# Kernel tuning notes

Measured on AMD Instinct MI355X. Metric: run time of the kernel, lower is better.

The kernel has to match this reference:

```python
import math
import jax, jax.numpy as jnp
import numpy as np

D_MODEL = 1024
NUM_HEADS = 16
D_HEAD = D_MODEL // NUM_HEADS  # 64
K_S = 32  # sparse top-k keys kept per query
B, N = 2, 2048


def setup_inputs() -> dict:
    key = jax.random.key(0)
    ks = jax.random.split(key, 9)
    s = 1.0 / math.sqrt(D_MODEL)
    return {
        "x": jax.random.normal(ks[0], (B, N, D_MODEL), dtype=jnp.float32),
        "Wq": jax.random.normal(ks[1], (D_MODEL, D_MODEL), dtype=jnp.float32) * s,
        "bq": jnp.zeros((D_MODEL,), dtype=jnp.float32),
        "Wk": jax.random.normal(ks[2], (D_MODEL, D_MODEL), dtype=jnp.float32) * s,
        "bk": jnp.zeros((D_MODEL,), dtype=jnp.float32),
        "Wv": jax.random.normal(ks[3], (D_MODEL, D_MODEL), dtype=jnp.float32) * s,
        "bv": jnp.zeros((D_MODEL,), dtype=jnp.float32),
        "Wo": jax.random.normal(ks[4], (D_MODEL, D_MODEL), dtype=jnp.float32) * s,
        "bo": jnp.zeros((D_MODEL,), dtype=jnp.float32),
    }


def _attn(x, Wq, bq, Wk, bk, Wv, bv, Wo, bo):
    b, n, _ = x.shape
    # projections (torch Linear: y = x W^T + b)
    q = (x @ Wq.T + bq).reshape(b, n, NUM_HEADS, D_HEAD).transpose(0, 2, 1, 3)
    k = (x @ Wk.T + bk).reshape(b, n, NUM_HEADS, D_HEAD).transpose(0, 2, 1, 3)
    v = (x @ Wv.T + bv).reshape(b, n, NUM_HEADS, D_HEAD).transpose(0, 2, 1, 3)
    # full scores [b, H, n, n]
    scores = jnp.einsum("bhqd,bhkd->bhqk", q, k) / math.sqrt(D_HEAD)
    # causal mask (triu above diagonal -> -inf)
    causal = jnp.triu(jnp.ones((n, n), dtype=bool), k=1)
    neg_inf = jnp.array(-jnp.inf, dtype=scores.dtype)
    scores = jnp.where(causal, neg_inf, scores)
    # sparse top-k: keep only K_S largest scores per query row
    vals, idx = jax.lax.top_k(scores, K_S)
    masked = jnp.full_like(scores, -jnp.inf)
    masked = jnp.put_along_axis(masked, idx, vals, axis=-1, inplace=False)
    attn = jax.nn.softmax(masked, axis=-1)  # dropout p=0.0 -> identity
    out = jnp.einsum("bhqk,bhkd->bhqd", attn, v)
    out = out.transpose(0, 2, 1, 3).reshape(b, n, D_MODEL)
    y = out @ Wo.T + bo
    return y, attn.mean(axis=1)


def reference(x, Wq, bq, Wk, bk, Wv, bv, Wo, bo):
    return _attn(x, Wq, bq, Wk, bk, Wv, bv, Wo, bo)
```

## Files before the change

kernel.cpp:

```cpp
#include <hip/hip_runtime.h>
#include <hip/hip_bf16.h>
#include <math.h>

#define BATCH   2
#define NTOK    2048
#define DMODEL  1024
#define HEADS   16
#define DHEAD   64
#define KSEL    32
#define MROWS   (BATCH * NTOK)

typedef short     bf16x8 __attribute__((ext_vector_type(8)));
typedef float     f32x4  __attribute__((ext_vector_type(4)));
typedef unsigned short ushort_t;
typedef unsigned long long u64;

#define GLOAD_LDS16(g, l) \
    __builtin_amdgcn_global_load_lds((const __attribute__((address_space(1))) void*)(g), \
                                     (__attribute__((address_space(3))) void*)(l), 16, 0, 0)

__device__ __forceinline__ ushort_t f2bf(float f) {
    unsigned u = __float_as_uint(f);
    unsigned r = (u + 0x7FFFu + ((u >> 16) & 1u)) >> 16;
    return (ushort_t)r;
}
__device__ __forceinline__ float bf2f(ushort_t h) {
    return __uint_as_float(((unsigned)h) << 16);
}

__global__ __launch_bounds__(256) void conv_split(const float* __restrict__ in,
                                                  ushort_t* __restrict__ hi,
                                                  ushort_t* __restrict__ lo, int n)
{
    const int i = (blockIdx.x * 256 + threadIdx.x) * 4;
    if (i + 3 < n) {
        const float4 v = *(const float4*)(in + i);
        ushort4 ph, pl;
        ph.x = f2bf(v.x); pl.x = f2bf(v.x - bf2f(ph.x));
        ph.y = f2bf(v.y); pl.y = f2bf(v.y - bf2f(ph.y));
        ph.z = f2bf(v.z); pl.z = f2bf(v.z - bf2f(ph.z));
        ph.w = f2bf(v.w); pl.w = f2bf(v.w - bf2f(ph.w));
        *(ushort4*)(hi + i) = ph;
        *(ushort4*)(lo + i) = pl;
    }
}

__global__ __launch_bounds__(256) void zero_fill(float* __restrict__ p, int n4)
{
    const int i = blockIdx.x * 256 + threadIdx.x;
    if (i < n4) ((float4*)p)[i] = (float4){0.f, 0.f, 0.f, 0.f};
}

__device__ __forceinline__ unsigned mono_key(float f) {
    const unsigned u = __float_as_uint(f);
    return (u ^ (unsigned)(((int)u >> 31) | 0x80000000)) + 1u;
}
__device__ __forceinline__ float unmono(unsigned m) {
    const unsigned u = m - 1u;
    return __uint_as_float(u ^ (unsigned)(((int)(~u) >> 31) | 0x80000000));
}

__global__ __launch_bounds__(256) void gemm_split_mfma(const ushort_t* __restrict__ Ahi,
                                                       const ushort_t* __restrict__ Alo,
                                                       const ushort_t* __restrict__ Bhi,
                                                       const ushort_t* __restrict__ Blo,
                                                       const float* __restrict__ bias,
                                                       float* __restrict__ out,
                                                       ushort_t* __restrict__ oh,
                                                       ushort_t* __restrict__ om,
                                                       ushort_t* __restrict__ ol,
                                                       int mode)
{
    __shared__ ushort_t AbufH[128 * 32];
    __shared__ ushort_t AbufL[128 * 32];
    __shared__ ushort_t BbufH[64 * 32];
    __shared__ ushort_t BbufL[64 * 32];

    const int tid  = threadIdx.x;
    const int wave = tid >> 6;
    const int lane = tid & 63;
    const int m0 = blockIdx.x * 128;
    const int n0 = blockIdx.y * 64;

    f32x4 acc[2][4];
#pragma unroll
    for (int i = 0; i < 2; ++i)
#pragma unroll
        for (int j = 0; j < 4; ++j) acc[i][j] = (f32x4){0.f, 0.f, 0.f, 0.f};

    const int ar0 = tid >> 2;
    const int ar1 = 64 + (tid >> 2);
    const int ak  = (tid & 3) << 3;
    const int br  = tid >> 2;

    const int fr = lane & 15;
    const int fk = (lane >> 4) << 3;

    for (int k0 = 0; k0 < DMODEL; k0 += 32) {
        __syncthreads();
        const size_t aoff0 = (size_t)(m0 + ar0) * DMODEL + k0 + ak;
        const size_t aoff1 = (size_t)(m0 + ar1) * DMODEL + k0 + ak;
        const size_t boff  = (size_t)(n0 + br) * DMODEL + k0 + ak;
        GLOAD_LDS16(Ahi + aoff0, AbufH + (size_t)tid * 8);
        GLOAD_LDS16(Ahi + aoff1, AbufH + (size_t)(256 + tid) * 8);
        GLOAD_LDS16(Alo + aoff0, AbufL + (size_t)tid * 8);
        GLOAD_LDS16(Alo + aoff1, AbufL + (size_t)(256 + tid) * 8);
        GLOAD_LDS16(Bhi + boff, BbufH + (size_t)tid * 8);
        GLOAD_LDS16(Blo + boff, BbufL + (size_t)tid * 8);
        __syncthreads();

        bf16x8 afh[2], afl[2], bfh[4], bfl[4];
#pragma unroll
        for (int mi = 0; mi < 2; ++mi) {
            const int ro = (wave * 32 + mi * 16 + fr) * 32 + fk;
            afh[mi] = *(const bf16x8*)(AbufH + ro);
            afl[mi] = *(const bf16x8*)(AbufL + ro);
        }
#pragma unroll
        for (int ni = 0; ni < 4; ++ni) {
            const int ro = (ni * 16 + fr) * 32 + fk;
            bfh[ni] = *(const bf16x8*)(BbufH + ro);
            bfl[ni] = *(const bf16x8*)(BbufL + ro);
        }

#pragma unroll
        for (int mi = 0; mi < 2; ++mi)
#pragma unroll
            for (int ni = 0; ni < 4; ++ni) {
                acc[mi][ni] = __builtin_amdgcn_mfma_f32_16x16x32_bf16(afh[mi], bfl[ni], acc[mi][ni], 0, 0, 0);
                acc[mi][ni] = __builtin_amdgcn_mfma_f32_16x16x32_bf16(afl[mi], bfh[ni], acc[mi][ni], 0, 0, 0);
                acc[mi][ni] = __builtin_amdgcn_mfma_f32_16x16x32_bf16(afh[mi], bfh[ni], acc[mi][ni], 0, 0, 0);
            }
    }

#pragma unroll
    for (int ni = 0; ni < 4; ++ni) {
        const int o = n0 + ni * 16 + (lane & 15);
        const float bv = bias[o];
#pragma unroll
        for (int mi = 0; mi < 2; ++mi) {
#pragma unroll
            for (int reg = 0; reg < 4; ++reg) {
                const int m = m0 + wave * 32 + mi * 16 + ((lane >> 4) << 2) + reg;
                const float v = acc[mi][ni][reg] + bv;
                if (mode == 0) {
                    out[(size_t)m * DMODEL + o] = v;
                } else {
                    const int bb = m >> 11;
                    const int n  = m & 2047;
                    const int hd = o >> 6;
                    const int d  = o & 63;
                    const size_t off = (((size_t)(bb * HEADS + hd)) * NTOK + n) * DHEAD + d;
                    if (mode == 1) {
                        out[off] = v;
                    } else {
                        const ushort_t h1 = f2bf(v);
                        const float r1 = v - bf2f(h1);
                        const ushort_t m1 = f2bf(r1);
                        const ushort_t l1 = f2bf(r1 - bf2f(m1));
                        oh[off] = h1; om[off] = m1; ol[off] = l1;
                    }
                }
            }
        }
    }
}

__global__ __launch_bounds__(256) void score_mfma(const ushort_t* __restrict__ Qh,
                                                  const ushort_t* __restrict__ Qm,
                                                  const ushort_t* __restrict__ Ql,
                                                  const ushort_t* __restrict__ Kh,
                                                  const ushort_t* __restrict__ Km,
                                                  const ushort_t* __restrict__ Kl,
                                                  unsigned* __restrict__ S,
                                                  int q0, int QC)
{
    const int kt = blockIdx.x;
    const int qt = blockIdx.y;
    const int bh = blockIdx.z;
    const int qbase = q0 + qt * 128;
    if (kt * 64 > qbase + 127) return;

    __shared__ ushort_t QhB[128 * 32], QmB[128 * 32], QlB[128 * 32];
    __shared__ ushort_t KhB[64 * 32],  KmB[64 * 32],  KlB[64 * 32];

    const int tid  = threadIdx.x;
    const int wave = tid >> 6;
    const int lane = tid & 63;

    const size_t qgbase = ((size_t)bh * NTOK + qbase) * DHEAD;
    const size_t kgbase = ((size_t)bh * NTOK + kt * 64) * DHEAD;

    f32x4 acc[2][4];
#pragma unroll
    for (int i = 0; i < 2; ++i)
#pragma unroll
        for (int j = 0; j < 4; ++j) acc[i][j] = (f32x4){0.f, 0.f, 0.f, 0.f};

#pragma unroll
    for (int kit = 0; kit < 2; ++kit) {
        const int koff = kit * 32;
        __syncthreads();
#pragma unroll
        for (int i = 0; i < 2; ++i) {
            const int c = i * 256 + tid;
            const int row = c >> 2;
            const int pos = (c & 3) ^ ((row >> 1) & 3);
            const size_t g = qgbase + (size_t)row * DHEAD + koff + pos * 8;
            GLOAD_LDS16(Qh + g, QhB + (size_t)c * 8);
            GLOAD_LDS16(Qm + g, QmB + (size_t)c * 8);
            GLOAD_LDS16(Ql + g, QlB + (size_t)c * 8);
        }
        {
            const int c = tid;
            const int row = c >> 2;
            const int pos = (c & 3) ^ ((row >> 1) & 3);
            const size_t g = kgbase + (size_t)row * DHEAD + koff + pos * 8;
            GLOAD_LDS16(Kh + g, KhB + (size_t)c * 8);
            GLOAD_LDS16(Km + g, KmB + (size_t)c * 8);
            GLOAD_LDS16(Kl + g, KlB + (size_t)c * 8);
        }
        __syncthreads();

        const int k8 = lane >> 4;

        bf16x8 qhf[2], qmf[2], qlf[2];
#pragma unroll
        for (int mi = 0; mi < 2; ++mi) {
            const int r = wave * 32 + mi * 16 + (lane & 15);
            const int ch = r * 4 + (k8 ^ ((r >> 1) & 3));
            qhf[mi] = *(const bf16x8*)(QhB + (size_t)ch * 8);
            qmf[mi] = *(const bf16x8*)(QmB + (size_t)ch * 8);
            qlf[mi] = *(const bf16x8*)(QlB + (size_t)ch * 8);
        }
        bf16x8 khf[4], kmf[4], klf[4];
#pragma unroll
        for (int ni = 0; ni < 4; ++ni) {
            const int r = ni * 16 + (lane & 15);
            const int ch = r * 4 + (k8 ^ ((r >> 1) & 3));
            khf[ni] = *(const bf16x8*)(KhB + (size_t)ch * 8);
            kmf[ni] = *(const bf16x8*)(KmB + (size_t)ch * 8);
            klf[ni] = *(const bf16x8*)(KlB + (size_t)ch * 8);
        }

#pragma unroll
        for (int mi = 0; mi < 2; ++mi)
#pragma unroll
            for (int ni = 0; ni < 4; ++ni) {
                acc[mi][ni] = __builtin_amdgcn_mfma_f32_16x16x32_bf16(qhf[mi], klf[ni], acc[mi][ni], 0, 0, 0);
                acc[mi][ni] = __builtin_amdgcn_mfma_f32_16x16x32_bf16(qlf[mi], khf[ni], acc[mi][ni], 0, 0, 0);
                acc[mi][ni] = __builtin_amdgcn_mfma_f32_16x16x32_bf16(qmf[mi], kmf[ni], acc[mi][ni], 0, 0, 0);
                acc[mi][ni] = __builtin_amdgcn_mfma_f32_16x16x32_bf16(qhf[mi], kmf[ni], acc[mi][ni], 0, 0, 0);
                acc[mi][ni] = __builtin_amdgcn_mfma_f32_16x16x32_bf16(qmf[mi], khf[ni], acc[mi][ni], 0, 0, 0);
                acc[mi][ni] = __builtin_amdgcn_mfma_f32_16x16x32_bf16(qhf[mi], khf[ni], acc[mi][ni], 0, 0, 0);
            }
    }

#pragma unroll
    for (int ni = 0; ni < 4; ++ni) {
        const int col = kt * 64 + ni * 16 + (lane & 15);
#pragma unroll
        for (int mi = 0; mi < 2; ++mi) {
#pragma unroll
            for (int reg = 0; reg < 4; ++reg) {
                const int mrow = wave * 32 + mi * 16 + ((lane >> 4) << 2) + reg;
                const int qlrow = qt * 128 + mrow;
                S[((size_t)bh * QC + qlrow) * NTOK + col] =
                    mono_key(acc[mi][ni][reg] * 0.125f);
            }
        }
    }
}

template<int SLOTS>
__device__ __forceinline__ void select_task(const unsigned* __restrict__ Srow,
                                            const float* __restrict__ Vb,
                                            float* __restrict__ ctxRow,
                                            float* __restrict__ attnRow,
                                            int L, int nsel,
                                            int* __restrict__ sIdx,
                                            float* __restrict__ sE)
{
    const int lane = threadIdx.x & 63;

    unsigned km[SLOTS];
    unsigned lmax = 0u;
#pragma unroll
    for (int s = 0; s < SLOTS; ++s) {
        const int j = s * 64 + lane;
        unsigned m = 0u;
        if (j < L) m = Srow[j];
        km[s] = m;
        lmax = (m > lmax) ? m : lmax;
    }

    unsigned gmax = lmax, mmin = lmax;
#pragma unroll
    for (int d = 1; d < 64; d <<= 1) {
        const unsigned o1 = __shfl_xor(gmax, d, 64);
        const unsigned o2 = __shfl_xor(mmin, d, 64);
        gmax = (o1 > gmax) ? o1 : gmax;
        mmin = (o2 < mmin) ? o2 : mmin;
    }

    unsigned lo = (L >= 64) ? (mmin >> 16) : 1u;
    if (lo < 1u) lo = 1u;
    unsigned hi = gmax >> 16;
    while (lo < hi) {
        const unsigned mid = lo + ((hi - lo + 1u) >> 1);
        const unsigned midk = mid << 16;
        int cnt = 0;
#pragma unroll
        for (int s = 0; s < SLOTS; ++s)
            cnt += __popcll(__ballot(km[s] >= midk));
        if (cnt >= nsel) lo = mid; else hi = mid - 1u;
    }
    const unsigned Tk  = lo << 16;
    const unsigned Gk  = Tk | 0xFFFFu;

    int cnt_ge = 0, cnt_gt = 0;
#pragma unroll
    for (int s = 0; s < SLOTS; ++s) {
        cnt_ge += __popcll(__ballot(km[s] >= Tk));
        cnt_gt += __popcll(__ballot(km[s] > Gk));
    }

    unsigned selmask = 0u;
    if (cnt_ge == nsel) {
#pragma unroll
        for (int s = 0; s < SLOTS; ++s)
            selmask |= (km[s] >= Tk) ? (1u << s) : 0u;
    } else {
        unsigned bmask = 0u;
#pragma unroll
        for (int s = 0; s < SLOTS; ++s) {
            selmask |= (km[s] > Gk) ? (1u << s) : 0u;
            bmask   |= (km[s] >= Tk && km[s] <= Gk) ? (1u << s) : 0u;
        }
        int k_tie = nsel - cnt_gt;
        while (k_tie > 0) {
            u64 best = 0;
            unsigned bm = bmask;
            while (bm) {
                const int s = __builtin_ctz(bm);
                bm &= bm - 1u;
                const u64 k = ((u64)km[s] << 32) | (unsigned)~(s * 64 + lane);
                if (k > best) best = k;
            }
            u64 b = best;
#pragma unroll
            for (int d = 1; d < 64; d <<= 1) {
                const u64 o = __shfl_xor(b, d, 64);
                b = (o > b) ? o : b;
            }
            const unsigned gidx = ~(unsigned)b;
            if (lane == (int)(gidx & 63u)) {
                const unsigned bit = 1u << (gidx >> 6);
                selmask |= bit;
                bmask &= ~bit;
            }
            --k_tie;
        }
    }

    const int c = __popc(selmask);
    int pfx = c;
#pragma unroll
    for (int d = 1; d < 64; d <<= 1) {
        const int t = __shfl_up(pfx, d, 64);
        if (lane >= d) pfx += t;
    }
    pfx -= c;

    const float vmax = unmono(gmax);
    float esum = 0.f;
    unsigned msk = selmask;
    int pos = pfx;
    while (msk) {
        const int s = __builtin_ctz(msk);
        msk &= msk - 1u;
        const int j = s * 64 + lane;
        const float e = __expf(unmono(km[s]) - vmax);
        esum += e;
        sIdx[pos] = j;
        sE[pos] = e;
        ++pos;
    }

    float Z = esum;
#pragma unroll
    for (int d = 1; d < 64; d <<= 1) Z += __shfl_xor(Z, d, 64);
    const float rcpZ = 1.0f / Z;

    msk = selmask;
    pos = pfx;
    while (msk) {
        const int s = __builtin_ctz(msk);
        msk &= msk - 1u;
        const int j = s * 64 + lane;
        const float w = sE[pos] * rcpZ;
        ++pos;
        atomicAdd(&attnRow[j], w * (1.0f / (float)HEADS));
    }

    float acc = 0.f;
    for (int i = 0; i < nsel; ++i) {
        const int idx = sIdx[i];
        const float wi = sE[i] * rcpZ;
        acc += wi * Vb[(size_t)idx * DHEAD + lane];
    }
    ctxRow[lane] = acc;
}

__global__ __launch_bounds__(256) void select_v5(const unsigned* __restrict__ S,
                                                 const float* __restrict__ V,
                                                 float* __restrict__ ctx,
                                                 float* __restrict__ attn,
                                                 int q0, int QC)
{
    __shared__ int   sIdxAll[4][KSEL];
    __shared__ float sEAll[4][KSEL];

    const int wave = threadIdx.x >> 6;
    const int ql = blockIdx.x;
    const int b  = blockIdx.y >> 2;
    const int hg = blockIdx.y & 3;
    const int h  = hg * 4 + wave;
    const int q  = q0 + ql;
    const int L = q + 1;
    const int nsel = (L < KSEL) ? L : KSEL;

    const size_t bh = (size_t)(b * HEADS + h);
    const unsigned* Srow = S + (bh * QC + ql) * NTOK;
    const float* Vb   = V + bh * NTOK * DHEAD;
    float* ctxRow  = ctx + (((size_t)(b * NTOK + q)) * HEADS + h) * DHEAD;
    float* attnRow = attn + ((size_t)(b * NTOK + q)) * NTOK;

    if (q < 512)       select_task<8 >(Srow, Vb, ctxRow, attnRow, L, nsel, sIdxAll[wave], sEAll[wave]);
    else if (q < 1024) select_task<16>(Srow, Vb, ctxRow, attnRow, L, nsel, sIdxAll[wave], sEAll[wave]);
    else               select_task<32>(Srow, Vb, ctxRow, attnRow, L, nsel, sIdxAll[wave], sEAll[wave]);
}

extern "C" void kernel_launch(void* const* d_in, const int* in_sizes, int n_in,
                              void* d_out, int out_size, void* d_ws, size_t ws_size,
                              hipStream_t stream) {
    const float* x  = (const float*)d_in[0];
    const float* Wq = (const float*)d_in[1];
    const float* bq = (const float*)d_in[2];
    const float* Wk = (const float*)d_in[3];
    const float* bk = (const float*)d_in[4];
    const float* Wv = (const float*)d_in[5];
    const float* bv = (const float*)d_in[6];
    const float* Wo = (const float*)d_in[7];
    const float* bo = (const float*)d_in[8];

    const size_t MB = 1ull << 20;
    char* wsb = (char*)d_ws;
    float*    Vws = (float*)(wsb + 0 * MB);
    float*    ctx = (float*)(wsb + 16 * MB);
    ushort_t* xhi = (ushort_t*)(wsb + 32 * MB);
    ushort_t* xlo = (ushort_t*)(wsb + 40 * MB);
    ushort_t* wqh = (ushort_t*)(wsb + 48 * MB);
    ushort_t* wql = (ushort_t*)(wsb + 50 * MB);
    ushort_t* wkh = (ushort_t*)(wsb + 52 * MB);
    ushort_t* wkl = (ushort_t*)(wsb + 54 * MB);
    ushort_t* wvh = (ushort_t*)(wsb + 56 * MB);
    ushort_t* wvl = (ushort_t*)(wsb + 58 * MB);
    ushort_t* woh = (ushort_t*)(wsb + 60 * MB);
    ushort_t* wol = (ushort_t*)(wsb + 62 * MB);
    ushort_t* Qh  = (ushort_t*)(wsb + 64 * MB);
    ushort_t* Qm  = (ushort_t*)(wsb + 72 * MB);
    ushort_t* Ql  = (ushort_t*)(wsb + 80 * MB);
    ushort_t* Kh  = (ushort_t*)(wsb + 88 * MB);
    ushort_t* Km  = (ushort_t*)(wsb + 96 * MB);
    ushort_t* Kl  = (ushort_t*)(wsb + 104 * MB);
    unsigned* Sws = (unsigned*)(wsb + 112 * MB);
    ushort_t* cxh = xhi;
    ushort_t* cxl = xlo;

    float* y    = (float*)d_out;
    float* attn = y + (size_t)BATCH * NTOK * DMODEL;

    const int NX = MROWS * DMODEL;
    const int NW = DMODEL * DMODEL;

    conv_split<<<NX / (256 * 4), 256, 0, stream>>>(x, xhi, xlo, NX);
    conv_split<<<NW / (256 * 4), 256, 0, stream>>>(Wq, wqh, wql, NW);
    conv_split<<<NW / (256 * 4), 256, 0, stream>>>(Wk, wkh, wkl, NW);
    conv_split<<<NW / (256 * 4), 256, 0, stream>>>(Wv, wvh, wvl, NW);
    conv_split<<<NW / (256 * 4), 256, 0, stream>>>(Wo, woh, wol, NW);

    dim3 ggrid(MROWS / 128, DMODEL / 64);
    gemm_split_mfma<<<ggrid, 256, 0, stream>>>(xhi, xlo, wqh, wql, bq, nullptr, Qh, Qm, Ql, 2);
    gemm_split_mfma<<<ggrid, 256, 0, stream>>>(xhi, xlo, wkh, wkl, bk, nullptr, Kh, Km, Kl, 2);
    gemm_split_mfma<<<ggrid, 256, 0, stream>>>(xhi, xlo, wvh, wvl, bv, Vws, nullptr, nullptr, nullptr, 1);

    const size_t base_bytes = 112 * MB;
    const size_t avail = (ws_size > base_bytes) ? ws_size - base_bytes : 0;
    int QC = 128;
    for (int cand = NTOK; cand >= 128; cand >>= 1) {
        const size_t need = (size_t)BATCH * HEADS * cand * NTOK * sizeof(unsigned);
        if (need <= avail) { QC = cand; break; }
    }

    const int nattn4 = BATCH * NTOK * NTOK / 4;
    zero_fill<<<(nattn4 + 255) / 256, 256, 0, stream>>>(attn, nattn4);
    for (int q0 = 0; q0 < NTOK; q0 += QC) {
        dim3 sgrid((q0 + QC) >> 6, QC / 128, BATCH * HEADS);
        score_mfma<<<sgrid, 256, 0, stream>>>(Qh, Qm, Ql, Kh, Km, Kl, Sws, q0, QC);
        dim3 selgrid(QC, BATCH * 4);
        select_v5<<<selgrid, 256, 0, stream>>>(Sws, Vws, ctx, attn, q0, QC);
    }

    conv_split<<<NX / (256 * 4), 256, 0, stream>>>(ctx, cxh, cxl, NX);
    gemm_split_mfma<<<ggrid, 256, 0, stream>>>(cxh, cxl, woh, wol, bo, y, nullptr, nullptr, nullptr, 0);
}
```

Baseline: 562.4 us.

## Prune top-k candidates using per-8-column block maxima computed in score kernel

The score kernel now also reduces each row's scores over groups of 8 columns and writes a per-block maximum. The selection kernel first picks the top 32 blocks by that maximum, then runs the exact top-32 search over only the 256 scores in those blocks. Before, it scanned the whole causal row of up to 2048 entries. This is meant to cut selection-kernel memory reads and ballot loops, at the cost of extra shuffles and stores in the score kernel, slightly less workspace for score chunks, and reworked tie-breaking.

```diff
diff --git a/kernel.cpp b/kernel.cpp
--- a/kernel.cpp
+++ b/kernel.cpp
@@ -9,6 +9,7 @@
 #define DHEAD   64
 #define KSEL    32
 #define MROWS   (BATCH * NTOK)
+#define NBLK8   (NTOK / 8)
 
 typedef short     bf16x8 __attribute__((ext_vector_type(8)));
 typedef float     f32x4  __attribute__((ext_vector_type(4)));
@@ -173,6 +174,7 @@
                                                   const ushort_t* __restrict__ Km,
                                                   const ushort_t* __restrict__ Kl,
                                                   unsigned* __restrict__ S,
+                                                  unsigned* __restrict__ Smax,
                                                   int q0, int QC)
 {
     const int kt = blockIdx.x;
@@ -265,180 +267,282 @@
             for (int reg = 0; reg < 4; ++reg) {
                 const int mrow = wave * 32 + mi * 16 + ((lane >> 4) << 2) + reg;
                 const int qlrow = qt * 128 + mrow;
-                S[((size_t)bh * QC + qlrow) * NTOK + col] =
-                    mono_key(acc[mi][ni][reg] * 0.125f);
-            }
-        }
-    }
-}
-
-template<int SLOTS>
-__device__ __forceinline__ void select_task(const unsigned* __restrict__ Srow,
-                                            const float* __restrict__ Vb,
-                                            float* __restrict__ ctxRow,
-                                            float* __restrict__ attnRow,
-                                            int L, int nsel,
-                                            int* __restrict__ sIdx,
-                                            float* __restrict__ sE)
-{
-    const int lane = threadIdx.x & 63;
-
-    unsigned km[SLOTS];
-    unsigned lmax = 0u;
-#pragma unroll
-    for (int s = 0; s < SLOTS; ++s) {
-        const int j = s * 64 + lane;
-        unsigned m = 0u;
-        if (j < L) m = Srow[j];
-        km[s] = m;
-        lmax = (m > lmax) ? m : lmax;
-    }
-
-    unsigned gmax = lmax, mmin = lmax;
-#pragma unroll
-    for (int d = 1; d < 64; d <<= 1) {
-        const unsigned o1 = __shfl_xor(gmax, d, 64);
-        const unsigned o2 = __shfl_xor(mmin, d, 64);
-        gmax = (o1 > gmax) ? o1 : gmax;
-        mmin = (o2 < mmin) ? o2 : mmin;
-    }
-
-    unsigned lo = (L >= 64) ? (mmin >> 16) : 1u;
-    if (lo < 1u) lo = 1u;
-    unsigned hi = gmax >> 16;
-    while (lo < hi) {
-        const unsigned mid = lo + ((hi - lo + 1u) >> 1);
-        const unsigned midk = mid << 16;
-        int cnt = 0;
-#pragma unroll
-        for (int s = 0; s < SLOTS; ++s)
-            cnt += __popcll(__ballot(km[s] >= midk));
-        if (cnt >= nsel) lo = mid; else hi = mid - 1u;
-    }
-    const unsigned Tk  = lo << 16;
-    const unsigned Gk  = Tk | 0xFFFFu;
-
-    int cnt_ge = 0, cnt_gt = 0;
-#pragma unroll
-    for (int s = 0; s < SLOTS; ++s) {
-        cnt_ge += __popcll(__ballot(km[s] >= Tk));
-        cnt_gt += __popcll(__ballot(km[s] > Gk));
-    }
-
-    unsigned selmask = 0u;
-    if (cnt_ge == nsel) {
-#pragma unroll
-        for (int s = 0; s < SLOTS; ++s)
-            selmask |= (km[s] >= Tk) ? (1u << s) : 0u;
-    } else {
-        unsigned bmask = 0u;
-#pragma unroll
-        for (int s = 0; s < SLOTS; ++s) {
-            selmask |= (km[s] > Gk) ? (1u << s) : 0u;
-            bmask   |= (km[s] >= Tk && km[s] <= Gk) ? (1u << s) : 0u;
-        }
-        int k_tie = nsel - cnt_gt;
-        while (k_tie > 0) {
-            u64 best = 0;
-            unsigned bm = bmask;
-            while (bm) {
-                const int s = __builtin_ctz(bm);
-                bm &= bm - 1u;
-                const u64 k = ((u64)km[s] << 32) | (unsigned)~(s * 64 + lane);
-                if (k > best) best = k;
-            }
-            u64 b = best;
-#pragma unroll
-            for (int d = 1; d < 64; d <<= 1) {
-                const u64 o = __shfl_xor(b, d, 64);
-                b = (o > b) ? o : b;
-            }
-            const unsigned gidx = ~(unsigned)b;
-            if (lane == (int)(gidx & 63u)) {
-                const unsigned bit = 1u << (gidx >> 6);
-                selmask |= bit;
-                bmask &= ~bit;
-            }
-            --k_tie;
-        }
-    }
-
-    const int c = __popc(selmask);
-    int pfx = c;
-#pragma unroll
-    for (int d = 1; d < 64; d <<= 1) {
-        const int t = __shfl_up(pfx, d, 64);
-        if (lane >= d) pfx += t;
-    }
-    pfx -= c;
-
-    const float vmax = unmono(gmax);
-    float esum = 0.f;
-    unsigned msk = selmask;
-    int pos = pfx;
-    while (msk) {
-        const int s = __builtin_ctz(msk);
-        msk &= msk - 1u;
-        const int j = s * 64 + lane;
-        const float e = __expf(unmono(km[s]) - vmax);
-        esum += e;
-        sIdx[pos] = j;
-        sE[pos] = e;
-        ++pos;
-    }
-
-    float Z = esum;
-#pragma unroll
-    for (int d = 1; d < 64; d <<= 1) Z += __shfl_xor(Z, d, 64);
-    const float rcpZ = 1.0f / Z;
-
-    msk = selmask;
-    pos = pfx;
-    while (msk) {
-        const int s = __builtin_ctz(msk);
-        msk &= msk - 1u;
-        const int j = s * 64 + lane;
-        const float w = sE[pos] * rcpZ;
-        ++pos;
-        atomicAdd(&attnRow[j], w * (1.0f / (float)HEADS));
-    }
-
-    float acc = 0.f;
-    for (int i = 0; i < nsel; ++i) {
-        const int idx = sIdx[i];
-        const float wi = sE[i] * rcpZ;
-        acc += wi * Vb[(size_t)idx * DHEAD + lane];
-    }
-    ctxRow[lane] = acc;
-}
-
-__global__ __launch_bounds__(256) void select_v5(const unsigned* __restrict__ S,
+                const int qglob = qbase + mrow;
+                const unsigned mk = mono_key(acc[mi][ni][reg] * 0.125f);
+                S[((size_t)bh * QC + qlrow) * NTOK + col] = mk;
+                unsigned cm = (col <= qglob) ? mk : 0u;
+                {
+                    unsigned o;
+                    o = __shfl_xor(cm, 1, 64); cm = (o > cm) ? o : cm;
+                    o = __shfl_xor(cm, 2, 64); cm = (o > cm) ? o : cm;
+                    o = __shfl_xor(cm, 4, 64); cm = (o > cm) ? o : cm;
+                }
+                if ((lane & 7) == 0) {
+                    const int gblk = kt * 8 + ni * 2 + ((lane >> 3) & 1);
+                    Smax[((size_t)bh * QC + qlrow) * NBLK8 + gblk] = cm;
+                }
+            }
+        }
+    }
+}
+
+__global__ __launch_bounds__(256) void select_v6(const unsigned* __restrict__ S,
+                                                 const unsigned* __restrict__ Smax,
                                                  const float* __restrict__ V,
                                                  float* __restrict__ ctx,
                                                  float* __restrict__ attn,
                                                  int q0, int QC)
 {
+    __shared__ int   sBlkAll[4][KSEL];
     __shared__ int   sIdxAll[4][KSEL];
     __shared__ float sEAll[4][KSEL];
 
+    const int lane = threadIdx.x & 63;
     const int wave = threadIdx.x >> 6;
     const int ql = blockIdx.x;
     const int b  = blockIdx.y >> 2;
     const int hg = blockIdx.y & 3;
     const int h  = hg * 4 + wave;
     const int q  = q0 + ql;
-    const int L = q + 1;
+    const int L  = q + 1;
     const int nsel = (L < KSEL) ? L : KSEL;
-
-    const size_t bh = (size_t)(b * HEADS + h);
-    const unsigned* Srow = S + (bh * QC + ql) * NTOK;
-    const float* Vb   = V + bh * NTOK * DHEAD;
+    const int nb = (L + 7) >> 3;
+
+    const size_t bhx = (size_t)(b * HEADS + h);
+    const unsigned* Srow = S + (bhx * QC + ql) * NTOK;
+    const unsigned* Mrow = Smax + (bhx * QC + ql) * NBLK8;
+    const float* Vb   = V + bhx * NTOK * DHEAD;
     float* ctxRow  = ctx + (((size_t)(b * NTOK + q)) * HEADS + h) * DHEAD;
     float* attnRow = attn + ((size_t)(b * NTOK + q)) * NTOK;
-
-    if (q < 512)       select_task<8 >(Srow, Vb, ctxRow, attnRow, L, nsel, sIdxAll[wave], sEAll[wave]);
-    else if (q < 1024) select_task<16>(Srow, Vb, ctxRow, attnRow, L, nsel, sIdxAll[wave], sEAll[wave]);
-    else               select_task<32>(Srow, Vb, ctxRow, attnRow, L, nsel, sIdxAll[wave], sEAll[wave]);
+    int*   sBlk = sBlkAll[wave];
+    int*   sIdx = sIdxAll[wave];
+    float* sE   = sEAll[wave];
+
+    const uint4 bm4 = *(const uint4*)(Mrow + lane * 4);
+    unsigned bmax[4] = {bm4.x, bm4.y, bm4.z, bm4.w};
+#pragma unroll
+    for (int s = 0; s < 4; ++s)
+        if (lane * 4 + s >= nb) bmax[s] = 0u;
+
+    unsigned gmax = bmax[0];
+    gmax = (bmax[1] > gmax) ? bmax[1] : gmax;
+    gmax = (bmax[2] > gmax) ? bmax[2] : gmax;
+    gmax = (bmax[3] > gmax) ? bmax[3] : gmax;
+#pragma unroll
+    for (int d = 1; d < 64; d <<= 1) {
+        const unsigned o = __shfl_xor(gmax, d, 64);
+        gmax = (o > gmax) ? o : gmax;
+    }
+    const float vmax = unmono(gmax);
+
+    unsigned selb = 0u;
+    unsigned blkLo = 1u;
+    int nselb;
+    if (nb <= KSEL) {
+        nselb = nb;
+#pragma unroll
+        for (int s = 0; s < 4; ++s)
+            if (lane * 4 + s < nb) selb |= 1u << s;
+    } else {
+        nselb = KSEL;
+        unsigned lo = 1u, hi = gmax >> 16;
+        while (lo < hi) {
+            const unsigned mid = lo + ((hi - lo + 1u) >> 1);
+            const unsigned midk = mid << 16;
+            int cnt = 0;
+#pragma unroll
+            for (int s = 0; s < 4; ++s)
+                cnt += __popcll(__ballot(bmax[s] >= midk));
+            if (cnt >= KSEL) lo = mid; else hi = mid - 1u;
+        }
+        blkLo = lo;
+        const unsigned Tkb = lo << 16;
+        const unsigned Gkb = Tkb | 0xFFFFu;
+        int cge = 0, cgt = 0;
+#pragma unroll
+        for (int s = 0; s < 4; ++s) {
+            cge += __popcll(__ballot(bmax[s] >= Tkb));
+            cgt += __popcll(__ballot(bmax[s] > Gkb));
+        }
+        if (cge == KSEL) {
+#pragma unroll
+            for (int s = 0; s < 4; ++s)
+                selb |= (bmax[s] >= Tkb) ? (1u << s) : 0u;
+        } else {
+            unsigned bmb = 0u;
+#pragma unroll
+            for (int s = 0; s < 4; ++s) {
+                selb |= (bmax[s] > Gkb) ? (1u << s) : 0u;
+                bmb  |= (bmax[s] >= Tkb && bmax[s] <= Gkb) ? (1u << s) : 0u;
+            }
+            int k_tie = KSEL - cgt;
+            while (k_tie > 0) {
+                u64 best = 0;
+                unsigned bmm = bmb;
+                while (bmm) {
+                    const int s = __builtin_ctz(bmm);
+                    bmm &= bmm - 1u;
+                    const unsigned gblk = (unsigned)(lane * 4 + s);
+                    const u64 k = ((u64)bmax[s] << 32) | (unsigned)~gblk;
+                    if (k > best) best = k;
+                }
+                u64 bb = best;
+#pragma unroll
+                for (int d = 1; d < 64; d <<= 1) {
+                    const u64 o = __shfl_xor(bb, d, 64);
+                    bb = (o > bb) ? o : bb;
+                }
+                const unsigned gblk = ~(unsigned)bb;
+                if (lane == (int)(gblk >> 2)) {
+                    const unsigned bit = 1u << (gblk & 3u);
+                    selb |= bit;
+                    bmb &= ~bit;
+                }
+                --k_tie;
+            }
+        }
+    }
+
+    {
+        const int cb = __popc(selb);
+        int pfxb = cb;
+#pragma unroll
+        for (int d = 1; d < 64; d <<= 1) {
+            const int t = __shfl_up(pfxb, d, 64);
+            if (lane >= d) pfxb += t;
+        }
+        pfxb -= cb;
+        unsigned mskb = selb;
+        int posb = pfxb;
+        while (mskb) {
+            const int s = __builtin_ctz(mskb);
+            mskb &= mskb - 1u;
+            sBlk[posb++] = lane * 4 + s;
+        }
+    }
+    __asm volatile("s_waitcnt lgkmcnt(0)" ::: "memory");
+
+    const int NC = nselb * 8;
+    unsigned km[4];
+    int idx[4];
+#pragma unroll
+    for (int c = 0; c < 4; ++c) {
+        const int t = c * 64 + lane;
+        unsigned m = 0u;
+        int j = 0;
+        if (t < NC) {
+            const int blk = sBlk[t >> 3];
+            j = blk * 8 + (t & 7);
+            if (j < L) m = Srow[j];
+        }
+        km[c] = m;
+        idx[c] = j;
+    }
+
+    unsigned lo = blkLo, hi = gmax >> 16;
+    while (lo < hi) {
+        const unsigned mid = lo + ((hi - lo + 1u) >> 1);
+        const unsigned midk = mid << 16;
+        int cnt = 0;
+#pragma unroll
+        for (int c = 0; c < 4; ++c)
+            cnt += __popcll(__ballot(km[c] >= midk));
+        if (cnt >= nsel) lo = mid; else hi = mid - 1u;
+    }
+    const unsigned Tk = lo << 16;
+    const unsigned Gk = Tk | 0xFFFFu;
+
+    int cnt_ge = 0, cnt_gt = 0;
+#pragma unroll
+    for (int c = 0; c < 4; ++c) {
+        cnt_ge += __popcll(__ballot(km[c] >= Tk));
+        cnt_gt += __popcll(__ballot(km[c] > Gk));
+    }
+
+    unsigned selmask = 0u;
+    if (cnt_ge == nsel) {
+#pragma unroll
+        for (int c = 0; c < 4; ++c)
+            selmask |= (km[c] >= Tk) ? (1u << c) : 0u;
+    } else {
+        unsigned bmask = 0u;
+#pragma unroll
+        for (int c = 0; c < 4; ++c) {
+            selmask |= (km[c] > Gk) ? (1u << c) : 0u;
+            bmask   |= (km[c] >= Tk && km[c] <= Gk) ? (1u << c) : 0u;
+        }
+        int k_tie = nsel - cnt_gt;
+        while (k_tie > 0) {
+            u64 best = 0;
+            unsigned bmm = bmask;
+            while (bmm) {
+                const int c = __builtin_ctz(bmm);
+                bmm &= bmm - 1u;
+                const int t = c * 64 + lane;
+                const u64 k = ((u64)km[c] << 32) |
+                              ((u64)(0xFFFFu ^ (unsigned)idx[c]) << 16) | (u64)t;
+                if (k > best) best = k;
+            }
+            u64 bb = best;
+#pragma unroll
+            for (int d = 1; d < 64; d <<= 1) {
+                const u64 o = __shfl_xor(bb, d, 64);
+                bb = (o > bb) ? o : bb;
+            }
+            const unsigned tt = (unsigned)bb & 0xFFFFu;
+            if (lane == (int)(tt & 63u)) {
+                const unsigned bit = 1u << (tt >> 6);
+                selmask |= bit;
+                bmask &= ~bit;
+            }
+            --k_tie;
+        }
+    }
+
+    const int csel = __popc(selmask);
+    int pfx = csel;
+#pragma unroll
+    for (int d = 1; d < 64; d <<= 1) {
+        const int t = __shfl_up(pfx, d, 64);
+        if (lane >= d) pfx += t;
+    }
+    pfx -= csel;
+
+    float esum = 0.f;
+    unsigned msk = selmask;
+    int pos = pfx;
+    while (msk) {
+        const int c = __builtin_ctz(msk);
+        msk &= msk - 1u;
+        const float e = __expf(unmono(km[c]) - vmax);
+        esum += e;
+        sIdx[pos] = idx[c];
+        sE[pos] = e;
+        ++pos;
+    }
+
+    float Z = esum;
+#pragma unroll
+    for (int d = 1; d < 64; d <<= 1) Z += __shfl_xor(Z, d, 64);
+    const float rcpZ = 1.0f / Z;
+
+    msk = selmask;
+    pos = pfx;
+    while (msk) {
+        const int c = __builtin_ctz(msk);
+        msk &= msk - 1u;
+        const float w = sE[pos] * rcpZ;
+        ++pos;
+        atomicAdd(&attnRow[idx[c]], w * (1.0f / (float)HEADS));
+    }
+
+    float acc = 0.f;
+    for (int i = 0; i < nsel; ++i) {
+        const int id = sIdx[i];
+        const float wi = sE[i] * rcpZ;
+        acc += wi * Vb[(size_t)id * DHEAD + lane];
+    }
+    ctxRow[lane] = acc;
 }
 
 extern "C" void kernel_launch(void* const* d_in, const int* in_sizes, int n_in,
@@ -474,7 +578,6 @@
     ushort_t* Kh  = (ushort_t*)(wsb + 88 * MB);
     ushort_t* Km  = (ushort_t*)(wsb + 96 * MB);
     ushort_t* Kl  = (ushort_t*)(wsb + 104 * MB);
-    unsigned* Sws = (unsigned*)(wsb + 112 * MB);
     ushort_t* cxh = xhi;
     ushort_t* cxl = xlo;
 
@@ -499,17 +602,20 @@
     const size_t avail = (ws_size > base_bytes) ? ws_size - base_bytes : 0;
     int QC = 128;
     for (int cand = NTOK; cand >= 128; cand >>= 1) {
-        const size_t need = (size_t)BATCH * HEADS * cand * NTOK * sizeof(unsigned);
+        const size_t need = (size_t)BATCH * HEADS * cand * (size_t)(NTOK + NBLK8) * sizeof(unsigned);
         if (need <= avail) { QC = cand; break; }
     }
+    unsigned* Smax = (unsigned*)(wsb + base_bytes);
+    unsigned* Sws  = (unsigned*)(wsb + base_bytes +
+                                 (size_t)BATCH * HEADS * QC * NBLK8 * sizeof(unsigned));
 
     const int nattn4 = BATCH * NTOK * NTOK / 4;
     zero_fill<<<(nattn4 + 255) / 256, 256, 0, stream>>>(attn, nattn4);
     for (int q0 = 0; q0 < NTOK; q0 += QC) {
         dim3 sgrid((q0 + QC) >> 6, QC / 128, BATCH * HEADS);
-        score_mfma<<<sgrid, 256, 0, stream>>>(Qh, Qm, Ql, Kh, Km, Kl, Sws, q0, QC);
+        score_mfma<<<sgrid, 256, 0, stream>>>(Qh, Qm, Ql, Kh, Km, Kl, Sws, Smax, q0, QC);
         dim3 selgrid(QC, BATCH * 4);
-        select_v5<<<selgrid, 256, 0, stream>>>(Sws, Vws, ctx, attn, q0, QC);
+        select_v6<<<selgrid, 256, 0, stream>>>(Sws, Smax, Vws, ctx, attn, q0, QC);
     }
 
     conv_split<<<NX / (256 * 4), 256, 0, stream>>>(ctx, cxh, cxl, NX);
```

After: 602.5 us. +7.1%, slower.
